# Kernel optimization log

Measured on AMD Instinct MI355X. Metric: run time of the kernel, lower is better.

The kernel has to match this reference:

```python
import jax, jax.numpy as jnp
import numpy as np

D = 64  # hidden size

def _ffn2(x, w1, b1, w2, b2):
    # Linear -> ReLU -> Linear (no activation after last layer, matching FFN)
    return jax.nn.relu(x @ w1 + b1) @ w2 + b2

def setup_inputs() -> dict:
    key = jax.random.key(0)
    ks = jax.random.split(key, 40)
    B, NP, NY, NO = 512, 128, 1024, 256
    f32 = jnp.float32
    def n(k, sh, s=0.1):
        return (jax.random.normal(k, sh) * s).astype(f32)
    inp = {
        'pred_state': jax.random.normal(ks[0], (B, NP, 2), dtype=f32),
        'prey_state': jax.random.normal(ks[1], (B, NY, 2), dtype=f32),
        'obst_state': jax.random.normal(ks[2], (B, NO, 3), dtype=f32),
        'prey_is_alive': jax.random.randint(ks[3], (B, NY), 0, 2).astype(bool),
        'emb': n(ks[4], (3, D)),
        'e0_w1': n(ks[5], (2, D)), 'e0_b1': n(ks[6], (D,)),
        'e0_w2': n(ks[7], (D, D)), 'e0_b2': n(ks[8], (D,)),
        'e1_w1': n(ks[9], (2, D)), 'e1_b1': n(ks[10], (D,)),
        'e1_w2': n(ks[11], (D, D)), 'e1_b2': n(ks[12], (D,)),
        'e2_w1': n(ks[13], (3, D)), 'e2_b1': n(ks[14], (D,)),
        'e2_w2': n(ks[15], (D, D)), 'e2_b2': n(ks[16], (D,)),
        'wq': n(ks[17], (D, D)), 'bq': n(ks[18], (D,)),
        'wk': n(ks[19], (D, D)), 'bk': n(ks[20], (D,)),
        'wv': n(ks[21], (D, D)), 'bv': n(ks[22], (D,)),
        'wp': n(ks[23], (2, D)), 'bp': n(ks[24], (D,)),
        'wo': n(ks[25], (D, D)), 'bo': n(ks[26], (D,)),
        'n_w1': n(ks[27], (D, D)), 'n_b1': n(ks[28], (D,)),
        'n_w2': n(ks[29], (D, D)), 'n_b2': n(ks[30], (D,)),
        'n_w3': n(ks[31], (D, 1), s=0.01), 'n_b3': n(ks[32], (1,)),
    }
    return inp

def reference(pred_state, prey_state, obst_state, prey_is_alive, emb,
              e0_w1, e0_b1, e0_w2, e0_b2,
              e1_w1, e1_b1, e1_w2, e1_b2,
              e2_w1, e2_b1, e2_w2, e2_b2,
              wq, bq, wk, bk, wv, bv, wp, bp, wo, bo,
              n_w1, n_b1, n_w2, n_b2, n_w3, n_b3):
    # per-entity encoders + type embedding
    x_pred = _ffn2(pred_state, e0_w1, e0_b1, e0_w2, e0_b2) + emb[0]  # [B,NP,D]
    x_prey = _ffn2(prey_state, e1_w1, e1_b1, e1_w2, e1_b2) + emb[1]  # [B,NY,D]
    x_obst = _ffn2(obst_state, e2_w1, e2_b1, e2_w2, e2_b2) + emb[2]  # [B,NO,D]
    x = jnp.concatenate([x_pred, x_prey, x_obst], axis=1)            # [B,N,D]
    pos = jnp.concatenate([pred_state, prey_state, obst_state[..., :2]], axis=1)  # [B,N,2]
    # NOTE: original mask = zeros.unsqueeze(-1) & (...) is identically False -> no masking.
    q = x_pred @ wq + bq   # [B,NP,D]
    k = x @ wk + bk        # [B,N,D]
    v = x @ wv + bv        # [B,N,D]
    # relative positional key bias: pbias = (pos_q - pos_k) @ wp; q . pbias folded as below
    qp = q @ wp.T          # [B,NP,2]
    scale = np.float32(1.0 / np.sqrt(D))
    scores = (jnp.einsum('bqd,bkd->bqk', q, k)
              + jnp.einsum('bqc,bqc->bq', qp, pred_state)[..., None]
              - jnp.einsum('bqc,bkc->bqk', qp, pos)
              + (q @ bp)[..., None]) * scale          # [B,NP,N]
    a = jax.nn.softmax(scores, axis=-1)
    out = jnp.einsum('bqk,bkd->bqd', a, v) @ wo + bo  # [B,NP,D]
    # output FFN with final Tanh
    h = jax.nn.relu(out @ n_w1 + n_b1)
    h = jax.nn.relu(h @ n_w2 + n_b2)
    return jnp.tanh(h @ n_w3 + n_b3)                  # [B,NP,1]
```

## Files before the change

### kernel.cpp

```cpp
#include <hip/hip_runtime.h>
#include <math.h>

#define NB 512
#define NPQ 128
#define NY 1024
#define NO 256
#define NTOT 1408
#define SCALE_E 0.180336884f

typedef __attribute__((ext_vector_type(8))) short bf16x8;
typedef __attribute__((ext_vector_type(4))) float f32x4;

__device__ __forceinline__ unsigned short f2bf(float f) {
    unsigned int u = __float_as_uint(f);
    u += 0x7fffu + ((u >> 16) & 1u);
    return (unsigned short)(u >> 16);
}
__device__ __forceinline__ float bf2f(short s) {
    return __uint_as_float(((unsigned int)(unsigned short)s) << 16);
}

union U8  { bf16x8 v; unsigned long long u[2]; };
union U16 { bf16x8 v; uint4 u; };

__global__ __launch_bounds__(256) void k_prepA(
    const float* __restrict__ emb,  const float* __restrict__ e0b2,
    const float* __restrict__ e0w2, const float* __restrict__ wq,
    const float* __restrict__ bq,   const float* __restrict__ wp,
    const float* __restrict__ bp,   const float* __restrict__ bk,
    const float* __restrict__ wvv,  const float* __restrict__ bv,
    const float* __restrict__ wo,   const float* __restrict__ bo,
    const float* __restrict__ e1b2, const float* __restrict__ e1w2,
    const float* __restrict__ e2b2, const float* __restrict__ e2w2,
    const float* __restrict__ nw1,  const float* __restrict__ nw2,
    float* __restrict__ W2qG, float* __restrict__ WvoG,
    float* __restrict__ scqG, float* __restrict__ b0g0,
    float* __restrict__ bvo,  float* __restrict__ BEP,
    unsigned short* __restrict__ W2P, unsigned short* __restrict__ WHP)
{
    const int tid = threadIdx.x, blk = blockIdx.x;

    if (blk < 16) {
        const int idx = blk*256 + tid;
        const int h = idx >> 6, j = idx & 63;
        float s0 = 0.f, s1 = 0.f, s2 = 0.f, s3 = 0.f;
        #pragma unroll 4
        for (int e = 0; e < 64; e += 4) {
            s0 = fmaf(e0w2[h*64+e],   wq[(e  )*64+j], s0);
            s1 = fmaf(e0w2[h*64+e+1], wq[(e+1)*64+j], s1);
            s2 = fmaf(e0w2[h*64+e+2], wq[(e+2)*64+j], s2);
            s3 = fmaf(e0w2[h*64+e+3], wq[(e+3)*64+j], s3);
        }
        W2qG[idx] = (s0 + s1) + (s2 + s3);
    } else if (blk < 32) {
        const int idx = (blk-16)*256 + tid;
        const int e = idx >> 6, o = idx & 63;
        float s0 = 0.f, s1 = 0.f, s2 = 0.f, s3 = 0.f;
        #pragma unroll 4
        for (int d = 0; d < 64; d += 4) {
            s0 = fmaf(wvv[e*64+d],   wo[(d  )*64+o], s0);
            s1 = fmaf(wvv[e*64+d+1], wo[(d+1)*64+o], s1);
            s2 = fmaf(wvv[e*64+d+2], wo[(d+2)*64+o], s2);
            s3 = fmaf(wvv[e*64+d+3], wo[(d+3)*64+o], s3);
        }
        WvoG[idx] = (s0 + s1) + (s2 + s3);
    } else if (blk < 38) {
        const int idx = (blk-32)*256 + tid;
        if (idx < 1536) {
            const int t = idx >> 9, rem = idx & 511;
            const int mt = rem >> 7, rem2 = rem & 127;
            const int kh = rem2 >> 6, lane = rem2 & 63;
            const int quad = lane >> 4, lq = lane & 15;
            const float* w2 = (t == 0) ? e0w2 : ((t == 1) ? e1w2 : e2w2);
            unsigned short v[8];
            #pragma unroll
            for (int j = 0; j < 8; ++j)
                v[j] = f2bf(w2[(kh*32 + quad*8 + j)*64 + mt*16 + lq]);
            *(uint4*)&W2P[(size_t)idx*8] = make_uint4(
                (unsigned int)v[0] | ((unsigned int)v[1] << 16),
                (unsigned int)v[2] | ((unsigned int)v[3] << 16),
                (unsigned int)v[4] | ((unsigned int)v[5] << 16),
                (unsigned int)v[6] | ((unsigned int)v[7] << 16));
        }
    } else if (blk < 42) {
        const int idx = 512 + (blk-38)*256 + tid;
        const int l = idx >> 9, rem = idx & 511;
        const int mt = rem >> 7, rem2 = rem & 127;
        const int kh = rem2 >> 6, lane = rem2 & 63;
        const int quad = lane >> 4, lq = lane & 15;
        const float* W = (l == 1) ? nw1 : nw2;
        unsigned short v[8];
        #pragma unroll
        for (int j = 0; j < 8; ++j)
            v[j] = f2bf(W[(kh*32 + quad*8 + j)*64 + mt*16 + lq]);
        *(uint4*)&WHP[(size_t)idx*8] = make_uint4(
            (unsigned int)v[0] | ((unsigned int)v[1] << 16),
            (unsigned int)v[2] | ((unsigned int)v[3] << 16),
            (unsigned int)v[4] | ((unsigned int)v[5] << 16),
            (unsigned int)v[6] | ((unsigned int)v[7] << 16));
    } else {
        __shared__ float scq[64];
        if (tid < 64) {
            const int j = tid;
            float s = bq[j];
            for (int e = 0; e < 64; ++e) s += (e0b2[e] + emb[e]) * wq[e*64+j];
            scq[j] = s;
            scqG[j] = s;
        }
        if (tid >= 64 && tid < 128) {
            const int o = tid - 64;
            float s = bo[o];
            for (int d = 0; d < 64; ++d) s += bv[d] * wo[d*64+o];
            bvo[o] = s;
        }
        {
            const int i = tid - 64;
            if (i >= 64 && i < 256) {
                const int idx = i - 64;
                const int t = idx >> 6, d = idx & 63;
                const float* b2 = (t == 0) ? e0b2 : ((t == 1) ? e1b2 : e2b2);
                BEP[idx] = b2[d] + emb[t*64 + d];
            }
        }
        __syncthreads();
        if (tid == 0) {
            float s0 = 0.f, s1 = 0.f, s2 = 0.f;
            for (int j = 0; j < 64; ++j) {
                s0 += scq[j] * wp[j];
                s1 += scq[j] * wp[64+j];
                s2 += scq[j] * (bp[j] + bk[j]);
            }
            b0g0[0] = SCALE_E * s0;
            b0g0[1] = SCALE_E * s1;
            b0g0[2] = SCALE_E * s2;
        }
    }
}

__global__ __launch_bounds__(256) void k_prepB(
    const float* __restrict__ W2qG, const float* __restrict__ WvoG,
    const float* __restrict__ scqG,
    const float* __restrict__ wk, const float* __restrict__ wp,
    const float* __restrict__ bp, const float* __restrict__ bk,
    unsigned short* __restrict__ AqkP, unsigned short* __restrict__ P3P,
    float* __restrict__ a0, unsigned short* __restrict__ WHP)
{
    const int tid = threadIdx.x, blk = blockIdx.x;

    if (blk < 2) {
        const int idx = blk*256 + tid;
        const int fi = idx >> 6, lane = idx & 63;
        const int mt = fi >> 1, kh = fi & 1;
        const int quad = lane >> 4, lq = lane & 15;
        const int d = mt*16 + lq;
        unsigned short v[8];
        #pragma unroll
        for (int jj = 0; jj < 8; ++jj) {
            const int h = kh*32 + quad*8 + jj;
            float s0 = 0.f, s1 = 0.f, s2 = 0.f, s3 = 0.f;
            #pragma unroll 4
            for (int j = 0; j < 64; j += 4) {
                const float4 a = *(const float4*)&W2qG[h*64 + j];
                const float4 b = *(const float4*)&wk[d*64 + j];
                s0 = fmaf(a.x, b.x, s0); s1 = fmaf(a.y, b.y, s1);
                s2 = fmaf(a.z, b.z, s2); s3 = fmaf(a.w, b.w, s3);
            }
            v[jj] = f2bf(SCALE_E * ((s0 + s1) + (s2 + s3)));
        }
        *(uint4*)&AqkP[(size_t)idx*8] = make_uint4(
            (unsigned int)v[0] | ((unsigned int)v[1] << 16),
            (unsigned int)v[2] | ((unsigned int)v[3] << 16),
            (unsigned int)v[4] | ((unsigned int)v[5] << 16),
            (unsigned int)v[6] | ((unsigned int)v[7] << 16));
    } else if (blk == 2) {
        if (tid < 128) {
            const int idx = tid;
            const int kh = idx >> 6, lane = idx & 63;
            const int quad = lane >> 4, lq = lane & 15;
            unsigned short v[8];
            #pragma unroll
            for (int jj = 0; jj < 8; ++jj) {
                const int h = kh*32 + quad*8 + jj;
                float val = 0.f;
                if (lq == 0 || lq == 1) {
                    float s0 = 0.f, s1 = 0.f;
                    #pragma unroll 8
                    for (int j = 0; j < 64; j += 2) {
                        s0 = fmaf(W2qG[h*64+j],   wp[lq*64+j],   s0);
                        s1 = fmaf(W2qG[h*64+j+1], wp[lq*64+j+1], s1);
                    }
                    val = s0 + s1;
                } else if (lq == 2) {
                    float s0 = 0.f, s1 = 0.f;
                    #pragma unroll 8
                    for (int j = 0; j < 64; j += 2) {
                        s0 = fmaf(W2qG[h*64+j],   bp[j]   + bk[j],   s0);
                        s1 = fmaf(W2qG[h*64+j+1], bp[j+1] + bk[j+1], s1);
                    }
                    val = s0 + s1;
                }
                v[jj] = f2bf(SCALE_E * val);
            }
            *(uint4*)&P3P[(size_t)idx*8] = make_uint4(
                (unsigned int)v[0] | ((unsigned int)v[1] << 16),
                (unsigned int)v[2] | ((unsigned int)v[3] << 16),
                (unsigned int)v[4] | ((unsigned int)v[5] << 16),
                (unsigned int)v[6] | ((unsigned int)v[7] << 16));
        } else if (tid < 192) {
            const int d = tid - 128;
            float s0 = 0.f, s1 = 0.f, s2 = 0.f, s3 = 0.f;
            #pragma unroll 4
            for (int j = 0; j < 64; j += 4) {
                const float4 a = *(const float4*)&scqG[j];
                const float4 b = *(const float4*)&wk[d*64 + j];
                s0 = fmaf(a.x, b.x, s0); s1 = fmaf(a.y, b.y, s1);
                s2 = fmaf(a.z, b.z, s2); s3 = fmaf(a.w, b.w, s3);
            }
            a0[d] = SCALE_E * ((s0 + s1) + (s2 + s3));
        }
    } else {
        #pragma unroll
        for (int pass = 0; pass < 2; ++pass) {
            const int idx = pass*256 + tid;
            const int mt = idx >> 7, rem2 = idx & 127;
            const int kh = rem2 >> 6, lane = rem2 & 63;
            const int quad = lane >> 4, lq = lane & 15;
            unsigned short v[8];
            #pragma unroll
            for (int j = 0; j < 8; ++j)
                v[j] = f2bf(WvoG[(kh*32 + quad*8 + j)*64 + mt*16 + lq]);
            *(uint4*)&WHP[(size_t)idx*8] = make_uint4(
                (unsigned int)v[0] | ((unsigned int)v[1] << 16),
                (unsigned int)v[2] | ((unsigned int)v[3] << 16),
                (unsigned int)v[4] | ((unsigned int)v[5] << 16),
                (unsigned int)v[6] | ((unsigned int)v[7] << 16));
        }
    }
}

__global__ __launch_bounds__(256) void k_encq(
    const float* __restrict__ pred, const float* __restrict__ prey,
    const float* __restrict__ obst,
    const unsigned short* __restrict__ W2P, const float* __restrict__ BEP,
    const float* __restrict__ e0w1, const float* __restrict__ e0b1,
    const float* __restrict__ e1w1, const float* __restrict__ e1b1,
    const float* __restrict__ e2w1, const float* __restrict__ e2b1,
    const unsigned short* __restrict__ AqkP, const float* __restrict__ a0,
    const unsigned short* __restrict__ P3P,  const float* __restrict__ b0g0,
    unsigned short* __restrict__ X, float* __restrict__ POS,
    float* __restrict__ QT, float* __restrict__ QP, float* __restrict__ QC)
{
    const int tid = threadIdx.x, lane = tid & 63, w = tid >> 6;
    const int lq = lane & 15, quad = lane >> 4;
    __shared__ __align__(16) short sH[4][32][68];

    if (blockIdx.x < 1408) {
        const int blk = blockIdx.x;
        int type, lrow0, cin, lsh, nmask, nbase;
        const float *st, *w1, *b1;
        if (blk < 128)       { type=0; lrow0=blk*512;         st=pred; w1=e0w1; b1=e0b1; cin=2; lsh=7;  nmask=NPQ-1; nbase=0; }
        else if (blk < 1152) { type=1; lrow0=(blk-128)*512;   st=prey; w1=e1w1; b1=e1b1; cin=2; lsh=10; nmask=NY-1;  nbase=NPQ; }
        else                 { type=2; lrow0=(blk-1152)*512;  st=obst; w1=e2w1; b1=e2b1; cin=3; lsh=8;  nmask=NO-1;  nbase=NPQ+NY; }

        bf16x8 wfrag[4][2];
        #pragma unroll
        for (int mt = 0; mt < 4; ++mt)
            #pragma unroll
            for (int kh = 0; kh < 2; ++kh)
                wfrag[mt][kh] = *(const bf16x8*)&W2P[(size_t)(((type*4 + mt)*2 + kh)*64 + lane)*8];

        float4 be[4];
        #pragma unroll
        for (int mt = 0; mt < 4; ++mt)
            be[mt] = *(const float4*)&BEP[type*64 + mt*16 + quad*4];

        float b1v[2][8], w0v[2][8], w1v[2][8], w2v[2][8];
        #pragma unroll
        for (int kh = 0; kh < 2; ++kh) {
            const int k0 = kh*32 + quad*8;
            *(float4*)&b1v[kh][0] = *(const float4*)&b1[k0];
            *(float4*)&b1v[kh][4] = *(const float4*)&b1[k0+4];
            *(float4*)&w0v[kh][0] = *(const float4*)&w1[k0];
            *(float4*)&w0v[kh][4] = *(const float4*)&w1[k0+4];
            *(float4*)&w1v[kh][0] = *(const float4*)&w1[64+k0];
            *(float4*)&w1v[kh][4] = *(const float4*)&w1[64+k0+4];
            if (cin == 3) {
                *(float4*)&w2v[kh][0] = *(const float4*)&w1[128+k0];
                *(float4*)&w2v[kh][4] = *(const float4*)&w1[128+k0+4];
            }
        }

        #pragma unroll
        for (int k = 0; k < 4; ++k) {
            const int i = tid*4 + k;
            const int r = i >> 1, c = i & 1;
            const int lr = lrow0 + r;
            const int pb = lr >> lsh, n = nbase + (lr & nmask);
            POS[((size_t)pb*NTOT + n)*2 + c] = st[(size_t)lr*cin + c];
        }

        for (int rt = 0; rt < 8; ++rt) {
            const int lr = lrow0 + w*128 + rt*16 + lq;
            float s0, s1, s2 = 0.f;
            if (cin == 2) {
                const float2 sv = *(const float2*)&st[(size_t)lr*2];
                s0 = sv.x; s1 = sv.y;
            } else {
                const float2 sv = *(const float2*)&st[(size_t)lr*3];
                s0 = sv.x; s1 = sv.y; s2 = st[(size_t)lr*3 + 2];
            }
            bf16x8 hb[2];
            #pragma unroll
            for (int kh = 0; kh < 2; ++kh)
                #pragma unroll
                for (int j = 0; j < 8; ++j) {
                    float a = b1v[kh][j] + s0*w0v[kh][j] + s1*w1v[kh][j];
                    if (cin == 3) a += s2*w2v[kh][j];
                    hb[kh][j] = (short)f2bf(fmaxf(a, 0.f));
                }

            f32x4 acc[4];
            #pragma unroll
            for (int mt = 0; mt < 4; ++mt) acc[mt] = (f32x4){0.f,0.f,0.f,0.f};
            #pragma unroll
            for (int mt = 0; mt < 4; ++mt) {
                acc[mt] = __builtin_amdgcn_mfma_f32_16x16x32_bf16(wfrag[mt][0], hb[0], acc[mt], 0, 0, 0);
                acc[mt] = __builtin_amdgcn_mfma_f32_16x16x32_bf16(wfrag[mt][1], hb[1], acc[mt], 0, 0, 0);
            }

            const int bb = lr >> lsh, n = nbase + (lr & nmask);
            unsigned short* xbase = X + ((size_t)bb*NTOT + n)*64;
            #pragma unroll
            for (int mt = 0; mt < 4; ++mt) {
                const unsigned int u0 = (unsigned int)f2bf(acc[mt][0] + be[mt].x)
                                      | ((unsigned int)f2bf(acc[mt][1] + be[mt].y) << 16);
                const unsigned int u1 = (unsigned int)f2bf(acc[mt][2] + be[mt].z)
                                      | ((unsigned int)f2bf(acc[mt][3] + be[mt].w) << 16);
                *(uint2*)(xbase + mt*16 + quad*4) = make_uint2(u0, u1);
            }
        }
    } else {
        const int b = blockIdx.x - 1408;
        const float w1r0 = e0w1[lane], w1r1 = e0w1[64+lane], b1r = e0b1[lane];
        {
            const float* sp = pred + ((size_t)b*NPQ + w*32)*2;
            #pragma unroll
            for (int r = 0; r < 32; ++r) {
                const float a = b1r + sp[2*r]*w1r0 + sp[2*r+1]*w1r1;
                sH[w][r][lane] = (short)f2bf(fmaxf(a, 0.f));
            }
        }

        bf16x8 wfrag[4][2], a3[2];
        #pragma unroll
        for (int mt = 0; mt < 4; ++mt)
            #pragma unroll
            for (int kh = 0; kh < 2; ++kh)
                wfrag[mt][kh] = *(const bf16x8*)&AqkP[(size_t)((mt*2 + kh)*64 + lane)*8];
        #pragma unroll
        for (int kh = 0; kh < 2; ++kh)
            a3[kh] = *(const bf16x8*)&P3P[(size_t)(kh*64 + lane)*8];

        float4 a0r[4];
        #pragma unroll
        for (int mt = 0; mt < 4; ++mt) a0r[mt] = *(const float4*)&a0[mt*16 + quad*4];
        const float c0 = b0g0[0], c1 = b0g0[1], c2 = b0g0[2];

        __syncthreads();

        for (int bt = 0; bt < 2; ++bt) {
            U8 hb0, hb1;
            const short* hp = &sH[w][bt*16 + lq][0];
            hb0.u[0] = *(const unsigned long long*)(hp + quad*8);
            hb0.u[1] = *(const unsigned long long*)(hp + quad*8 + 4);
            hb1.u[0] = *(const unsigned long long*)(hp + 32 + quad*8);
            hb1.u[1] = *(const unsigned long long*)(hp + 32 + quad*8 + 4);

            f32x4 acc[4], acc3;
            #pragma unroll
            for (int mt = 0; mt < 4; ++mt) acc[mt] = (f32x4){0.f,0.f,0.f,0.f};
            acc3 = (f32x4){0.f,0.f,0.f,0.f};
            #pragma unroll
            for (int mt = 0; mt < 4; ++mt) {
                acc[mt] = __builtin_amdgcn_mfma_f32_16x16x32_bf16(wfrag[mt][0], hb0.v, acc[mt], 0, 0, 0);
                acc[mt] = __builtin_amdgcn_mfma_f32_16x16x32_bf16(wfrag[mt][1], hb1.v, acc[mt], 0, 0, 0);
            }
            acc3 = __builtin_amdgcn_mfma_f32_16x16x32_bf16(a3[0], hb0.v, acc3, 0, 0, 0);
            acc3 = __builtin_amdgcn_mfma_f32_16x16x32_bf16(a3[1], hb1.v, acc3, 0, 0, 0);

            const int row = b*NPQ + w*32 + bt*16 + lq;
            #pragma unroll
            for (int mt = 0; mt < 4; ++mt) {
                *(float4*)&QT[(size_t)row*64 + mt*16 + quad*4] = make_float4(
                    acc[mt][0] + a0r[mt].x, acc[mt][1] + a0r[mt].y,
                    acc[mt][2] + a0r[mt].z, acc[mt][3] + a0r[mt].w);
            }
            if (quad == 0) {
                const float qp0 = acc3[0] + c0, qp1 = acc3[1] + c1, qs = acc3[2] + c2;
                const float p0 = pred[(size_t)row*2], p1 = pred[(size_t)row*2 + 1];
                QP[(size_t)row*2]     = qp0;
                QP[(size_t)row*2 + 1] = qp1;
                QC[row] = qp0*p0 + qp1*p1 + qs;
            }
        }
    }
}

__global__ __launch_bounds__(256, 4) void k_attn(
    const unsigned short* __restrict__ X, const float* __restrict__ POS,
    const float* __restrict__ QT, const float* __restrict__ QP,
    const float* __restrict__ QC,
    const unsigned short* __restrict__ WHP,
    const float* __restrict__ bvo, const float* __restrict__ nb1,
    const float* __restrict__ nb2,
    const float* __restrict__ nw3, const float* __restrict__ nb3,
    float* __restrict__ OUT)
{
    const int tid = threadIdx.x, b = blockIdx.x;
    const int w = tid >> 6, lane = tid & 63, lq = lane & 15, quad = lane >> 4;

    __shared__ __align__(16) char smem[34816 + 256];
    short (*sXc)[64][68] = (short (*)[64][68])(smem);
    short (*sP )[32][68] = (short (*)[32][68])(smem + 17408);
    short (*sA )[68]     = (short (*)[68])(smem);
    short (*sB )[68]     = (short (*)[68])(smem + 17408);
    float* sw3           = (float*)(smem + 34816);

    bf16x8 aq[2][2];
    #pragma unroll
    for (int qt = 0; qt < 2; ++qt) {
        const float* qrow = QT + ((size_t)b*NPQ + w*32 + qt*16 + lq)*64;
        #pragma unroll
        for (int kh = 0; kh < 2; ++kh)
            #pragma unroll
            for (int j = 0; j < 8; ++j)
                aq[qt][kh][j] = (short)f2bf(qrow[kh*32 + quad*8 + j]);
    }

    float qp0r[2][4], qp1r[2][4], lacc[2][4];
    f32x4 qcv[2];
    f32x4 O[2][4];
    #pragma unroll
    for (int qt = 0; qt < 2; ++qt)
        #pragma unroll
        for (int i = 0; i < 4; ++i) {
            const size_t g = (size_t)b*NPQ + w*32 + qt*16 + quad*4 + i;
            qcv[qt][i]  = QC[g];
            qp0r[qt][i] = -QP[2*g];
            qp1r[qt][i] = -QP[2*g+1];
            lacc[qt][i] = 0.f;
        }
    #pragma unroll
    for (int qt = 0; qt < 2; ++qt)
        #pragma unroll
        for (int nt = 0; nt < 4; ++nt) O[qt][nt] = (f32x4){0.f,0.f,0.f,0.f};

    const int skey = tid & 63, sd0 = (tid >> 6) * 16;

    for (int kt = 0; kt < 22; ++kt) {
        const int par = kt & 1;

        const unsigned short* gx = X + ((size_t)b*NTOT + kt*64 + skey)*64 + sd0;
        const uint4 t0 = *(const uint4*)(gx);
        const uint4 t1 = *(const uint4*)(gx + 8);

        if (kt > 0) {
            const int pb = par ^ 1;
            #pragma unroll
            for (int kc = 0; kc < 2; ++kc) {
                U8 pa[2];
                #pragma unroll
                for (int qt = 0; qt < 2; ++qt) {
                    const short* pp = &sP[w][qt*16 + lq][kc*32 + quad*8];
                    pa[qt].u[0] = *(const unsigned long long*)pp;
                    pa[qt].u[1] = *(const unsigned long long*)(pp + 4);
                }
                #pragma unroll
                for (int nt = 0; nt < 4; ++nt) {
                    U8 bv;
                    const short* xp = &sXc[pb][nt*16 + lq][kc*32 + quad*8];
                    bv.u[0] = *(const unsigned long long*)xp;
                    bv.u[1] = *(const unsigned long long*)(xp + 4);
                    O[0][nt] = __builtin_amdgcn_mfma_f32_16x16x32_bf16(pa[0].v, bv.v, O[0][nt], 0, 0, 0);
                    O[1][nt] = __builtin_amdgcn_mfma_f32_16x16x32_bf16(pa[1].v, bv.v, O[1][nt], 0, 0, 0);
                }
            }
        }

        __builtin_amdgcn_sched_barrier(0);

        #pragma unroll
        for (int nt = 0; nt < 4; ++nt) {
            U16 bx0, bx1;
            const unsigned short* xrow = X + ((size_t)b*NTOT + kt*64 + nt*16 + lq)*64;
            bx0.u = *(const uint4*)(xrow + quad*8);
            bx1.u = *(const uint4*)(xrow + 32 + quad*8);
            const float pos0 = POS[((size_t)b*NTOT + kt*64 + nt*16 + lq)*2];
            const float pos1 = POS[((size_t)b*NTOT + kt*64 + nt*16 + lq)*2 + 1];
            #pragma unroll
            for (int qt = 0; qt < 2; ++qt) {
                f32x4 sa = qcv[qt];
                sa = __builtin_amdgcn_mfma_f32_16x16x32_bf16(aq[qt][0], bx0.v, sa, 0, 0, 0);
                sa = __builtin_amdgcn_mfma_f32_16x16x32_bf16(aq[qt][1], bx1.v, sa, 0, 0, 0);
                #pragma unroll
                for (int i = 0; i < 4; ++i) {
                    float s = sa[i];
                    s = fmaf(qp0r[qt][i], pos0, s);
                    s = fmaf(qp1r[qt][i], pos1, s);
                    const float p = exp2f(s);
                    lacc[qt][i] += p;
                    sP[w][qt*16 + quad*4 + i][nt*16 + lq] = (short)f2bf(p);
                }
            }
        }

        {
            unsigned short tmp[16];
            *(uint4*)tmp = t0; *(uint4*)(tmp+8) = t1;
            #pragma unroll
            for (int j = 0; j < 16; ++j) sXc[par][sd0+j][skey] = (short)tmp[j];
        }

        __syncthreads();
    }

    {
        #pragma unroll
        for (int kc = 0; kc < 2; ++kc) {
            U8 pa[2];
            #pragma unroll
            for (int qt = 0; qt < 2; ++qt) {
                const short* pp = &sP[w][qt*16 + lq][kc*32 + quad*8];
                pa[qt].u[0] = *(const unsigned long long*)pp;
                pa[qt].u[1] = *(const unsigned long long*)(pp + 4);
            }
            #pragma unroll
            for (int nt = 0; nt < 4; ++nt) {
                U8 bv;
                const short* xp = &sXc[1][nt*16 + lq][kc*32 + quad*8];
                bv.u[0] = *(const unsigned long long*)xp;
                bv.u[1] = *(const unsigned long long*)(xp + 4);
                O[0][nt] = __builtin_amdgcn_mfma_f32_16x16x32_bf16(pa[0].v, bv.v, O[0][nt], 0, 0, 0);
                O[1][nt] = __builtin_amdgcn_mfma_f32_16x16x32_bf16(pa[1].v, bv.v, O[1][nt], 0, 0, 0);
            }
        }
    }

    __syncthreads();

    #pragma unroll
    for (int qt = 0; qt < 2; ++qt)
        #pragma unroll
        for (int i = 0; i < 4; ++i) {
            #pragma unroll
            for (int off = 1; off < 16; off <<= 1)
                lacc[qt][i] += __shfl_xor(lacc[qt][i], off);
            const float rl = 1.f / lacc[qt][i];
            const int row = w*32 + qt*16 + quad*4 + i;
            #pragma unroll
            for (int nt = 0; nt < 4; ++nt)
                sA[row][nt*16 + lq] = (short)f2bf(O[qt][nt][i] * rl);
        }
    if (tid < 64) sw3[tid] = nw3[tid];
    __syncthreads();

    const float* Bs[3] = {bvo, nb1, nb2};
    for (int l = 0; l < 3; ++l) {
        bf16x8 wfrag[4][2];
        #pragma unroll
        for (int mt = 0; mt < 4; ++mt)
            #pragma unroll
            for (int kh = 0; kh < 2; ++kh)
                wfrag[mt][kh] = *(const bf16x8*)&WHP[(size_t)(((l*4 + mt)*2 + kh)*64 + lane)*8];
        const float* Bb = Bs[l];
        float be[4][4];
        #pragma unroll
        for (int mt = 0; mt < 4; ++mt)
            #pragma unroll
            for (int i = 0; i < 4; ++i) be[mt][i] = Bb[mt*16 + quad*4 + i];

        short (*src)[68] = (l & 1) ? sB : sA;
        short (*dst)[68] = (l & 1) ? sA : sB;
        const bool doRelu = (l >= 1);

        for (int bt = 0; bt < 2; ++bt) {
            U8 hb0, hb1;
            const short* hp = &src[w*32 + bt*16 + lq][0];
            hb0.u[0] = *(const unsigned long long*)(hp + quad*8);
            hb0.u[1] = *(const unsigned long long*)(hp + quad*8 + 4);
            hb1.u[0] = *(const unsigned long long*)(hp + 32 + quad*8);
            hb1.u[1] = *(const unsigned long long*)(hp + 32 + quad*8 + 4);

            f32x4 acc[4];
            #pragma unroll
            for (int mt = 0; mt < 4; ++mt) acc[mt] = (f32x4){0.f,0.f,0.f,0.f};
            #pragma unroll
            for (int mt = 0; mt < 4; ++mt) {
                acc[mt] = __builtin_amdgcn_mfma_f32_16x16x32_bf16(wfrag[mt][0], hb0.v, acc[mt], 0, 0, 0);
                acc[mt] = __builtin_amdgcn_mfma_f32_16x16x32_bf16(wfrag[mt][1], hb1.v, acc[mt], 0, 0, 0);
            }
            const int row = w*32 + bt*16 + lq;
            #pragma unroll
            for (int mt = 0; mt < 4; ++mt) {
                float v0 = acc[mt][0] + be[mt][0];
                float v1 = acc[mt][1] + be[mt][1];
                float v2 = acc[mt][2] + be[mt][2];
                float v3 = acc[mt][3] + be[mt][3];
                if (doRelu) {
                    v0 = fmaxf(v0, 0.f); v1 = fmaxf(v1, 0.f);
                    v2 = fmaxf(v2, 0.f); v3 = fmaxf(v3, 0.f);
                }
                const unsigned int u0 = (unsigned int)f2bf(v0) | ((unsigned int)f2bf(v1) << 16);
                const unsigned int u1 = (unsigned int)f2bf(v2) | ((unsigned int)f2bf(v3) << 16);
                *(uint2*)&dst[row][mt*16 + quad*4] = make_uint2(u0, u1);
            }
        }
        __syncthreads();
    }

    if (tid < 128) {
        const int row = tid;
        float acc = nb3[0];
        #pragma unroll 16
        for (int d = 0; d < 64; ++d) acc += bf2f(sB[row][d]) * sw3[d];
        OUT[(size_t)b*NPQ + row] = tanhf(acc);
    }
}

extern "C" void kernel_launch(void* const* d_in, const int* in_sizes, int n_in,
                              void* d_out, int out_size, void* d_ws, size_t ws_size,
                              hipStream_t stream)
{
    const float* pred = (const float*)d_in[0];
    const float* prey = (const float*)d_in[1];
    const float* obst = (const float*)d_in[2];
    const float* emb  = (const float*)d_in[4];
    const float* e0w1 = (const float*)d_in[5];
    const float* e0b1 = (const float*)d_in[6];
    const float* e0w2 = (const float*)d_in[7];
    const float* e0b2 = (const float*)d_in[8];
    const float* e1w1 = (const float*)d_in[9];
    const float* e1b1 = (const float*)d_in[10];
    const float* e1w2 = (const float*)d_in[11];
    const float* e1b2 = (const float*)d_in[12];
    const float* e2w1 = (const float*)d_in[13];
    const float* e2b1 = (const float*)d_in[14];
    const float* e2w2 = (const float*)d_in[15];
    const float* e2b2 = (const float*)d_in[16];
    const float* wq  = (const float*)d_in[17];
    const float* bq  = (const float*)d_in[18];
    const float* wk  = (const float*)d_in[19];
    const float* bk  = (const float*)d_in[20];
    const float* wvv = (const float*)d_in[21];
    const float* bv  = (const float*)d_in[22];
    const float* wp  = (const float*)d_in[23];
    const float* bp  = (const float*)d_in[24];
    const float* wo  = (const float*)d_in[25];
    const float* bo  = (const float*)d_in[26];
    const float* nw1 = (const float*)d_in[27];
    const float* nb1 = (const float*)d_in[28];
    const float* nw2 = (const float*)d_in[29];
    const float* nb2 = (const float*)d_in[30];
    const float* nw3 = (const float*)d_in[31];
    const float* nb3 = (const float*)d_in[32];

    char* ws = (char*)d_ws;
    unsigned short* X = (unsigned short*)ws;
    float* F    = (float*)(ws + 92274688);
    float* POS  = F;
    float* QT   = POS + 1441792;
    float* QP   = QT  + 4194304;
    float* QC   = QP  + 131072;
    float* a0   = QC  + 65536;
    float* b0g0 = a0  + 64;
    float* bvo  = b0g0 + 4;
    float* BEP  = bvo + 64;
    float* W2qG = BEP + 192;
    float* WvoG = W2qG + 4096;
    float* scqG = WvoG + 4096;
    unsigned short* W2P  = (unsigned short*)(scqG + 64);
    unsigned short* AqkP = W2P + 12288;
    unsigned short* P3P  = AqkP + 4096;
    unsigned short* WHP  = P3P + 1024;

    k_prepA<<<43, 256, 0, stream>>>(emb, e0b2, e0w2, wq, bq, wp, bp, bk,
        wvv, bv, wo, bo, e1b2, e1w2, e2b2, e2w2, nw1, nw2,
        W2qG, WvoG, scqG, b0g0, bvo, BEP, W2P, WHP);
    k_prepB<<<4, 256, 0, stream>>>(W2qG, WvoG, scqG, wk, wp, bp, bk,
        AqkP, P3P, a0, WHP);
    k_encq<<<1920, 256, 0, stream>>>(pred, prey, obst, W2P, BEP,
        e0w1, e0b1, e1w1, e1b1, e2w1, e2b1,
        AqkP, a0, P3P, b0g0, X, POS, QT, QP, QC);
    k_attn<<<512, 256, 0, stream>>>(X, POS, QT, QP, QC,
        WHP, bvo, nb1, nb2, nw3, nb3, (float*)d_out);
}
```

Measured before the change: 301.5 us.

## Split attention kernel across two blocks per batch by query halves

k_attn now launches two blocks per batch element, each owning 64 of the 128 query rows (16 per wave instead of 32). Per-block registers and shared memory shrink and the grid doubles, which should fill the GPU better than 512 blocks. The cost is that each block streams the full key/value tile set for its batch, so global reads of X and POS double. Launch bounds were relaxed to allow more registers.

```diff
diff --git a/kernel.cpp b/kernel.cpp
--- a/kernel.cpp
+++ b/kernel.cpp
@@ -406,7 +406,7 @@
     }
 }
 
-__global__ __launch_bounds__(256, 4) void k_attn(
+__global__ __launch_bounds__(256, 2) void k_attn(
     const unsigned short* __restrict__ X, const float* __restrict__ POS,
     const float* __restrict__ QT, const float* __restrict__ QP,
     const float* __restrict__ QC,
@@ -416,44 +416,41 @@
     const float* __restrict__ nw3, const float* __restrict__ nb3,
     float* __restrict__ OUT)
 {
-    const int tid = threadIdx.x, b = blockIdx.x;
+    const int tid = threadIdx.x;
+    const int b = blockIdx.x >> 1, qh = blockIdx.x & 1;
     const int w = tid >> 6, lane = tid & 63, lq = lane & 15, quad = lane >> 4;
-
-    __shared__ __align__(16) char smem[34816 + 256];
+    const int q0 = qh*64 + w*16;
+
+    __shared__ __align__(16) char smem[26112 + 256];
     short (*sXc)[64][68] = (short (*)[64][68])(smem);
-    short (*sP )[32][68] = (short (*)[32][68])(smem + 17408);
+    short (*sP )[16][68] = (short (*)[16][68])(smem + 17408);
     short (*sA )[68]     = (short (*)[68])(smem);
-    short (*sB )[68]     = (short (*)[68])(smem + 17408);
-    float* sw3           = (float*)(smem + 34816);
-
-    bf16x8 aq[2][2];
+    short (*sB )[68]     = (short (*)[68])(smem + 8704);
+    float* sw3           = (float*)(smem + 26112);
+
+    bf16x8 aq[2];
+    {
+        const float* qrow = QT + ((size_t)b*NPQ + q0 + lq)*64;
+        #pragma unroll
+        for (int kh = 0; kh < 2; ++kh)
+            #pragma unroll
+            for (int j = 0; j < 8; ++j)
+                aq[kh][j] = (short)f2bf(qrow[kh*32 + quad*8 + j]);
+    }
+
+    float qp0r[4], qp1r[4], lacc[4];
+    f32x4 qcv;
+    f32x4 O[4];
     #pragma unroll
-    for (int qt = 0; qt < 2; ++qt) {
-        const float* qrow = QT + ((size_t)b*NPQ + w*32 + qt*16 + lq)*64;
-        #pragma unroll
-        for (int kh = 0; kh < 2; ++kh)
-            #pragma unroll
-            for (int j = 0; j < 8; ++j)
-                aq[qt][kh][j] = (short)f2bf(qrow[kh*32 + quad*8 + j]);
-    }
-
-    float qp0r[2][4], qp1r[2][4], lacc[2][4];
-    f32x4 qcv[2];
-    f32x4 O[2][4];
+    for (int i = 0; i < 4; ++i) {
+        const size_t g = (size_t)b*NPQ + q0 + quad*4 + i;
+        qcv[i]  = QC[g];
+        qp0r[i] = -QP[2*g];
+        qp1r[i] = -QP[2*g+1];
+        lacc[i] = 0.f;
+    }
     #pragma unroll
-    for (int qt = 0; qt < 2; ++qt)
-        #pragma unroll
-        for (int i = 0; i < 4; ++i) {
-            const size_t g = (size_t)b*NPQ + w*32 + qt*16 + quad*4 + i;
-            qcv[qt][i]  = QC[g];
-            qp0r[qt][i] = -QP[2*g];
-            qp1r[qt][i] = -QP[2*g+1];
-            lacc[qt][i] = 0.f;
-        }
-    #pragma unroll
-    for (int qt = 0; qt < 2; ++qt)
-        #pragma unroll
-        for (int nt = 0; nt < 4; ++nt) O[qt][nt] = (f32x4){0.f,0.f,0.f,0.f};
+    for (int nt = 0; nt < 4; ++nt) O[nt] = (f32x4){0.f,0.f,0.f,0.f};
 
     const int skey = tid & 63, sd0 = (tid >> 6) * 16;
 
@@ -468,21 +465,17 @@
             const int pb = par ^ 1;
             #pragma unroll
             for (int kc = 0; kc < 2; ++kc) {
-                U8 pa[2];
-                #pragma unroll
-                for (int qt = 0; qt < 2; ++qt) {
-                    const short* pp = &sP[w][qt*16 + lq][kc*32 + quad*8];
-                    pa[qt].u[0] = *(const unsigned long long*)pp;
-                    pa[qt].u[1] = *(const unsigned long long*)(pp + 4);
-                }
+                U8 pa;
+                const short* pp = &sP[w][lq][kc*32 + quad*8];
+                pa.u[0] = *(const unsigned long long*)pp;
+                pa.u[1] = *(const unsigned long long*)(pp + 4);
                 #pragma unroll
                 for (int nt = 0; nt < 4; ++nt) {
                     U8 bv;
                     const short* xp = &sXc[pb][nt*16 + lq][kc*32 + quad*8];
                     bv.u[0] = *(const unsigned long long*)xp;
                     bv.u[1] = *(const unsigned long long*)(xp + 4);
-                    O[0][nt] = __builtin_amdgcn_mfma_f32_16x16x32_bf16(pa[0].v, bv.v, O[0][nt], 0, 0, 0);
-                    O[1][nt] = __builtin_amdgcn_mfma_f32_16x16x32_bf16(pa[1].v, bv.v, O[1][nt], 0, 0, 0);
+                    O[nt] = __builtin_amdgcn_mfma_f32_16x16x32_bf16(pa.v, bv.v, O[nt], 0, 0, 0);
                 }
             }
         }
@@ -497,20 +490,17 @@
             bx1.u = *(const uint4*)(xrow + 32 + quad*8);
             const float pos0 = POS[((size_t)b*NTOT + kt*64 + nt*16 + lq)*2];
             const float pos1 = POS[((size_t)b*NTOT + kt*64 + nt*16 + lq)*2 + 1];
-            #pragma unroll
-            for (int qt = 0; qt < 2; ++qt) {
-                f32x4 sa = qcv[qt];
-                sa = __builtin_amdgcn_mfma_f32_16x16x32_bf16(aq[qt][0], bx0.v, sa, 0, 0, 0);
-                sa = __builtin_amdgcn_mfma_f32_16x16x32_bf16(aq[qt][1], bx1.v, sa, 0, 0, 0);
-                #pragma unroll
-                for (int i = 0; i < 4; ++i) {
-                    float s = sa[i];
-                    s = fmaf(qp0r[qt][i], pos0, s);
-                    s = fmaf(qp1r[qt][i], pos1, s);
-                    const float p = exp2f(s);
-                    lacc[qt][i] += p;
-                    sP[w][qt*16 + quad*4 + i][nt*16 + lq] = (short)f2bf(p);
-                }
+            f32x4 sa = qcv;
+            sa = __builtin_amdgcn_mfma_f32_16x16x32_bf16(aq[0], bx0.v, sa, 0, 0, 0);
+            sa = __builtin_amdgcn_mfma_f32_16x16x32_bf16(aq[1], bx1.v, sa, 0, 0, 0);
+            #pragma unroll
+            for (int i = 0; i < 4; ++i) {
+                float s = sa[i];
+                s = fmaf(qp0r[i], pos0, s);
+                s = fmaf(qp1r[i], pos1, s);
+                const float p = exp2f(s);
+                lacc[i] += p;
+                sP[w][quad*4 + i][nt*16 + lq] = (short)f2bf(p);
             }
         }
 
@@ -527,40 +517,32 @@
     {
         #pragma unroll
         for (int kc = 0; kc < 2; ++kc) {
-            U8 pa[2];
-            #pragma unroll
-            for (int qt = 0; qt < 2; ++qt) {
-                const short* pp = &sP[w][qt*16 + lq][kc*32 + quad*8];
-                pa[qt].u[0] = *(const unsigned long long*)pp;
-                pa[qt].u[1] = *(const unsigned long long*)(pp + 4);
-            }
+            U8 pa;
+            const short* pp = &sP[w][lq][kc*32 + quad*8];
+            pa.u[0] = *(const unsigned long long*)pp;
+            pa.u[1] = *(const unsigned long long*)(pp + 4);
             #pragma unroll
             for (int nt = 0; nt < 4; ++nt) {
                 U8 bv;
                 const short* xp = &sXc[1][nt*16 + lq][kc*32 + quad*8];
                 bv.u[0] = *(const unsigned long long*)xp;
                 bv.u[1] = *(const unsigned long long*)(xp + 4);
-                O[0][nt] = __builtin_amdgcn_mfma_f32_16x16x32_bf16(pa[0].v, bv.v, O[0][nt], 0, 0, 0);
-                O[1][nt] = __builtin_amdgcn_mfma_f32_16x16x32_bf16(pa[1].v, bv.v, O[1][nt], 0, 0, 0);
-            }
-        }
-    }
-
-    __syncthreads();
+                O[nt] = __builtin_amdgcn_mfma_f32_16x16x32_bf16(pa.v, bv.v, O[nt], 0, 0, 0);
+            }
+        }
+    }
 
     #pragma unroll
-    for (int qt = 0; qt < 2; ++qt)
-        #pragma unroll
-        for (int i = 0; i < 4; ++i) {
-            #pragma unroll
-            for (int off = 1; off < 16; off <<= 1)
-                lacc[qt][i] += __shfl_xor(lacc[qt][i], off);
-            const float rl = 1.f / lacc[qt][i];
-            const int row = w*32 + qt*16 + quad*4 + i;
-            #pragma unroll
-            for (int nt = 0; nt < 4; ++nt)
-                sA[row][nt*16 + lq] = (short)f2bf(O[qt][nt][i] * rl);
-        }
+    for (int i = 0; i < 4; ++i) {
+        #pragma unroll
+        for (int off = 1; off < 16; off <<= 1)
+            lacc[i] += __shfl_xor(lacc[i], off);
+        const float rl = 1.f / lacc[i];
+        const int row = w*16 + quad*4 + i;
+        #pragma unroll
+        for (int nt = 0; nt < 4; ++nt)
+            sA[row][nt*16 + lq] = (short)f2bf(O[nt][i] * rl);
+    }
     if (tid < 64) sw3[tid] = nw3[tid];
     __syncthreads();
 
@@ -583,47 +565,45 @@
         short (*dst)[68] = (l & 1) ? sA : sB;
         const bool doRelu = (l >= 1);
 
-        for (int bt = 0; bt < 2; ++bt) {
-            U8 hb0, hb1;
-            const short* hp = &src[w*32 + bt*16 + lq][0];
-            hb0.u[0] = *(const unsigned long long*)(hp + quad*8);
-            hb0.u[1] = *(const unsigned long long*)(hp + quad*8 + 4);
-            hb1.u[0] = *(const unsigned long long*)(hp + 32 + quad*8);
-            hb1.u[1] = *(const unsigned long long*)(hp + 32 + quad*8 + 4);
-
-            f32x4 acc[4];
-            #pragma unroll
-            for (int mt = 0; mt < 4; ++mt) acc[mt] = (f32x4){0.f,0.f,0.f,0.f};
-            #pragma unroll
-            for (int mt = 0; mt < 4; ++mt) {
-                acc[mt] = __builtin_amdgcn_mfma_f32_16x16x32_bf16(wfrag[mt][0], hb0.v, acc[mt], 0, 0, 0);
-                acc[mt] = __builtin_amdgcn_mfma_f32_16x16x32_bf16(wfrag[mt][1], hb1.v, acc[mt], 0, 0, 0);
-            }
-            const int row = w*32 + bt*16 + lq;
-            #pragma unroll
-            for (int mt = 0; mt < 4; ++mt) {
-                float v0 = acc[mt][0] + be[mt][0];
-                float v1 = acc[mt][1] + be[mt][1];
-                float v2 = acc[mt][2] + be[mt][2];
-                float v3 = acc[mt][3] + be[mt][3];
-                if (doRelu) {
-                    v0 = fmaxf(v0, 0.f); v1 = fmaxf(v1, 0.f);
-                    v2 = fmaxf(v2, 0.f); v3 = fmaxf(v3, 0.f);
-                }
-                const unsigned int u0 = (unsigned int)f2bf(v0) | ((unsigned int)f2bf(v1) << 16);
-                const unsigned int u1 = (unsigned int)f2bf(v2) | ((unsigned int)f2bf(v3) << 16);
-                *(uint2*)&dst[row][mt*16 + quad*4] = make_uint2(u0, u1);
-            }
+        U8 hb0, hb1;
+        const short* hp = &src[w*16 + lq][0];
+        hb0.u[0] = *(const unsigned long long*)(hp + quad*8);
+        hb0.u[1] = *(const unsigned long long*)(hp + quad*8 + 4);
+        hb1.u[0] = *(const unsigned long long*)(hp + 32 + quad*8);
+        hb1.u[1] = *(const unsigned long long*)(hp + 32 + quad*8 + 4);
+
+        f32x4 acc[4];
+        #pragma unroll
+        for (int mt = 0; mt < 4; ++mt) acc[mt] = (f32x4){0.f,0.f,0.f,0.f};
+        #pragma unroll
+        for (int mt = 0; mt < 4; ++mt) {
+            acc[mt] = __builtin_amdgcn_mfma_f32_16x16x32_bf16(wfrag[mt][0], hb0.v, acc[mt], 0, 0, 0);
+            acc[mt] = __builtin_amdgcn_mfma_f32_16x16x32_bf16(wfrag[mt][1], hb1.v, acc[mt], 0, 0, 0);
+        }
+        const int row = w*16 + lq;
+        #pragma unroll
+        for (int mt = 0; mt < 4; ++mt) {
+            float v0 = acc[mt][0] + be[mt][0];
+            float v1 = acc[mt][1] + be[mt][1];
+            float v2 = acc[mt][2] + be[mt][2];
+            float v3 = acc[mt][3] + be[mt][3];
+            if (doRelu) {
+                v0 = fmaxf(v0, 0.f); v1 = fmaxf(v1, 0.f);
+                v2 = fmaxf(v2, 0.f); v3 = fmaxf(v3, 0.f);
+            }
+            const unsigned int u0 = (unsigned int)f2bf(v0) | ((unsigned int)f2bf(v1) << 16);
+            const unsigned int u1 = (unsigned int)f2bf(v2) | ((unsigned int)f2bf(v3) << 16);
+            *(uint2*)&dst[row][mt*16 + quad*4] = make_uint2(u0, u1);
         }
         __syncthreads();
     }
 
-    if (tid < 128) {
+    if (tid < 64) {
         const int row = tid;
         float acc = nb3[0];
         #pragma unroll 16
         for (int d = 0; d < 64; ++d) acc += bf2f(sB[row][d]) * sw3[d];
-        OUT[(size_t)b*NPQ + row] = tanhf(acc);
+        OUT[(size_t)b*NPQ + qh*64 + row] = tanhf(acc);
     }
 }
 
@@ -691,6 +671,6 @@
     k_encq<<<1920, 256, 0, stream>>>(pred, prey, obst, W2P, BEP,
         e0w1, e0b1, e1w1, e1b1, e2w1, e2b1,
         AqkP, a0, P3P, b0g0, X, POS, QT, QP, QC);
-    k_attn<<<512, 256, 0, stream>>>(X, POS, QT, QP, QC,
+    k_attn<<<1024, 256, 0, stream>>>(X, POS, QT, QP, QC,
         WHP, bvo, nb1, nb2, nw3, nb3, (float*)d_out);
 }
```

New measurement: 302.1 us. Within noise of the previous version (+0.2%).
